# Optimization experiments

Hardware: AMD Instinct MI355X
Metric: run time of the kernel (lower is better)

## Reference

```python
import jax, jax.numpy as jnp
import numpy as np

GN_GROUPS = 32
GN_EPS = 1e-5


def conv3x3(x, w, b=None):
    # x: [B,C,H,W], w: [O,I,3,3]
    y = jax.lax.conv_general_dilated(x, w, (1, 1), 'SAME',
                                     dimension_numbers=('NCHW', 'OIHW', 'NCHW'))
    if b is not None:
        y = y + b[None, :, None, None]
    return y


def group_norm(x, gamma, beta):
    B, C, H, W = x.shape
    xg = x.reshape(B, GN_GROUPS, C // GN_GROUPS, H, W)
    mu = xg.mean(axis=(2, 3, 4), keepdims=True)
    var = ((xg - mu) ** 2).mean(axis=(2, 3, 4), keepdims=True)
    xn = ((xg - mu) * jax.lax.rsqrt(var + GN_EPS)).reshape(B, C, H, W)
    return xn * gamma[None, :, None, None] + beta[None, :, None, None]


def tower(x, ws, gammas, betas):
    # ws: [n_conv, C, C, 3, 3]; conv(bias=False) -> GroupNorm -> ReLU, n_conv times
    for i in range(ws.shape[0]):
        x = jax.nn.relu(group_norm(conv3x3(x, ws[i]), gammas[i], betas[i]))
    return x


def setup_inputs() -> dict:
    key = jax.random.key(0)
    ks = jax.random.split(key, 20)
    C, n_conv, n_fg = 256, 4, 20  # n_class - 1 = 20
    prior = 0.01
    B = 2
    sizes = [(100, 100), (50, 50), (25, 25), (13, 13), (7, 7)]
    inp = {}
    for i, (h, w) in enumerate(sizes):
        inp[f'feat{i}'] = jax.random.normal(ks[i], (B, C, h, w), dtype=jnp.float32)
    std = 0.01  # init_conv_std
    inp['cls_tw_w'] = std * jax.random.normal(ks[5], (n_conv, C, C, 3, 3), dtype=jnp.float32)
    inp['cls_tw_g'] = jnp.ones((n_conv, C), dtype=jnp.float32)
    inp['cls_tw_b'] = jnp.zeros((n_conv, C), dtype=jnp.float32)
    inp['box_tw_w'] = std * jax.random.normal(ks[6], (n_conv, C, C, 3, 3), dtype=jnp.float32)
    inp['box_tw_g'] = jnp.ones((n_conv, C), dtype=jnp.float32)
    inp['box_tw_b'] = jnp.zeros((n_conv, C), dtype=jnp.float32)
    inp['cls_pred_w'] = std * jax.random.normal(ks[7], (n_fg, C, 3, 3), dtype=jnp.float32)
    prior_bias = -np.log((1.0 - prior) / prior)
    inp['cls_pred_b'] = jnp.full((n_fg,), prior_bias, dtype=jnp.float32)
    inp['box_pred_w'] = std * jax.random.normal(ks[8], (4, C, 3, 3), dtype=jnp.float32)
    inp['box_pred_b'] = jnp.zeros((4,), dtype=jnp.float32)
    inp['ctr_pred_w'] = std * jax.random.normal(ks[9], (1, C, 3, 3), dtype=jnp.float32)
    inp['ctr_pred_b'] = jnp.zeros((1,), dtype=jnp.float32)
    inp['scales'] = jnp.ones((5,), dtype=jnp.float32)
    return inp


def reference(feat0, feat1, feat2, feat3, feat4,
              cls_tw_w, cls_tw_g, cls_tw_b,
              box_tw_w, box_tw_g, box_tw_b,
              cls_pred_w, cls_pred_b,
              box_pred_w, box_pred_b,
              ctr_pred_w, ctr_pred_b,
              scales):
    feats = [feat0, feat1, feat2, feat3, feat4]
    logits, bboxes, centers = [], [], []
    for i, feat in enumerate(feats):
        c = tower(feat, cls_tw_w, cls_tw_g, cls_tw_b)
        logits.append(conv3x3(c, cls_pred_w, cls_pred_b))
        centers.append(conv3x3(c, ctr_pred_w, ctr_pred_b))
        b = tower(feat, box_tw_w, box_tw_g, box_tw_b)
        bboxes.append(jnp.exp(conv3x3(b, box_pred_w, box_pred_b) * scales[i]))
    return tuple(logits + bboxes + centers)
```

## Files before the change

### kernel.cpp

```cpp
#include <hip/hip_runtime.h>
#include <hip/hip_bf16.h>
#include <cstdint>

typedef unsigned short u16;
typedef __attribute__((ext_vector_type(8))) short short8;
typedef __attribute__((ext_vector_type(4))) float floatx4;
typedef __attribute__((ext_vector_type(4))) int intx4;

#define PA_TOTAL 13696
#define CCH 256
#define KTOT 2304

struct Tables {
  int H[5], W[5], P[5], base[5], tile0[5];
  int lb[5], bb[5], cb[5];
};
struct FeatPtrs { const float* f[5]; };
struct ConvArgs {
  const u16* X[2];
  const u16* Wt[2];
  u16* outB[2];
  float* stats;
  float* dout;
  const float* biasCls; const float* biasCtr; const float* biasBox; const float* scales;
};
struct ReorderArgs {
  const float* cls_w; const float* box_w; const float* pcls_w; const float* ctr_w; const float* pbox_w;
  u16* wrCls; u16* wrBox; u16* wrPCls; u16* wrPBox;
};

__device__ __forceinline__ u16 f2bf(float f) {
  union { float f; unsigned u; } v; v.f = f;
  unsigned r = v.u + 0x7fffu + ((v.u >> 16) & 1u);
  return (u16)(r >> 16);
}
__device__ __forceinline__ float bf2f(u16 h) {
  union { unsigned u; float f; } v; v.u = ((unsigned)h) << 16;
  return v.f;
}

__device__ __forceinline__ void gload16(const void* g, void* l) {
  __builtin_amdgcn_global_load_lds(
      (const __attribute__((address_space(1))) void*)g,
      (__attribute__((address_space(3))) void*)l, 16, 0, 0);
}

__global__ void reorder_all(ReorderArgs ra) {
  __shared__ float row[KTOT];
  const int r = blockIdx.x;
  const float* s;
  u16* o;
  if (r < 1024)      { s = ra.cls_w  + (size_t)r * KTOT;          o = ra.wrCls  + (size_t)r * KTOT; }
  else if (r < 2048) { int q = r - 1024; s = ra.box_w  + (size_t)q * KTOT; o = ra.wrBox  + (size_t)q * KTOT; }
  else if (r < 2068) { int q = r - 2048; s = ra.pcls_w + (size_t)q * KTOT; o = ra.wrPCls + (size_t)q * KTOT; }
  else if (r == 2068){ s = ra.ctr_w;                               o = ra.wrPCls + (size_t)20 * KTOT; }
  else if (r < 2073) { int q = r - 2069; s = ra.pbox_w + (size_t)q * KTOT; o = ra.wrPBox + (size_t)q * KTOT; }
  else if (r < 2084) {
    u16* oz = ra.wrPCls + (size_t)(21 + (r - 2073)) * KTOT;
#pragma unroll
    for (int j = 0; j < 9; ++j) oz[threadIdx.x + j * 256] = 0;
    return;
  } else {
    u16* oz = ra.wrPBox + (size_t)(4 + (r - 2084)) * KTOT;
#pragma unroll
    for (int j = 0; j < 9; ++j) oz[threadIdx.x + j * 256] = 0;
    return;
  }
#pragma unroll
  for (int j = 0; j < 9; ++j) row[threadIdx.x + j * 256] = s[threadIdx.x + j * 256];
  __syncthreads();
#pragma unroll
  for (int j = 0; j < 9; ++j) {
    int k = threadIdx.x + j * 256;
    o[k] = f2bf(row[(k & 255) * 9 + (k >> 8)]);
  }
}

__global__ void convert_inputs(FeatPtrs fp, u16* __restrict__ out, Tables tb) {
  __shared__ float tile[32][33];
  const int pt = blockIdx.x, c32 = blockIdx.y, b = blockIdx.z;
  const int p0 = pt * 32;
  int lvl = 0;
#pragma unroll
  for (int i = 1; i < 5; ++i) if (p0 >= tb.base[i]) lvl = i;
  const int P = tb.P[lvl];
  const int pl0 = p0 - tb.base[lvl];
  const int r = threadIdx.x >> 5, col = threadIdx.x & 31;
  const float* src = fp.f[lvl] + ((size_t)b * CCH + c32 * 32) * P;
#pragma unroll
  for (int i = 0; i < 4; ++i) {
    int crow = r + i * 8;
    int pl = pl0 + col;
    tile[crow][col] = (pl < P) ? src[(size_t)crow * P + pl] : 0.f;
  }
  __syncthreads();
#pragma unroll
  for (int i = 0; i < 4; ++i) {
    int px = r + i * 8;
    out[((size_t)b * PA_TOTAL + p0 + px) * CCH + c32 * 32 + col] = f2bf(tile[col][px]);
  }
}

template <int MODE>
__global__ __launch_bounds__(256) void conv_mfma(ConvArgs a, Tables tb) {
  constexpr int NI = (MODE == 0) ? 4 : 1;
  constexpr int WROWS = (MODE == 0) ? 128 : 32;
  const int L = blockIdx.x + (MODE == 0 ? 107 : 108) * (blockIdx.y + 2 * blockIdx.z);
  const int xcd = L & 7, slot = L >> 3;
  int tower, mt, b, t;
  if (MODE == 0) {
    tower = xcd >> 2; mt = (xcd >> 1) & 1; b = xcd & 1; t = slot;
  } else {
    tower = xcd >> 2; mt = 0; b = (xcd >> 1) & 1; t = slot * 2 + (xcd & 1);
    if (t >= 107) return;
  }
  int lvl = 0;
#pragma unroll
  for (int i = 1; i < 5; ++i) if (t >= tb.tile0[i]) lvl = i;
  const int H = tb.H[lvl], W = tb.W[lvl], P = tb.P[lvl], base = tb.base[lvl];
  const int n0 = (t - tb.tile0[lvl]) * 128;

  const int tid = threadIdx.x;
  const int lane = tid & 63, wv = tid >> 6;
  const int wm = wv >> 1, wn = wv & 1;

  __shared__ u16 ldsAll[128 * 64 + WROWS * 64];
  u16* ldsX = ldsAll;
  u16* ldsW = ldsAll + 128 * 64;

  const u16* X = a.X[tower];
  const u16* Wt = a.Wt[tower];
  const char* Xb = (const char*)(X + ((size_t)b * PA_TOTAL + base) * CCH);
  const char* Wb = (const char*)(Wt + (size_t)(MODE == 0 ? mt * 128 : 0) * KTOT);

  const int qsw2 = ((lane & 7) ^ (lane >> 3)) * 16;
  int xoffG[4];
  unsigned mask9[4];
  int xlds[4];
#pragma unroll
  for (int t4 = 0; t4 < 4; ++t4) {
    int row = (t4 * 4 + wv) * 8 + (lane >> 3);
    int prow = n0 + row;
    int rr = prow / W, cc = prow - rr * W;
    unsigned m = 0;
#pragma unroll
    for (int tap = 0; tap < 9; ++tap) {
      const int dh = tap / 3 - 1, dw = tap % 3 - 1;
      bool v = ((unsigned)(rr + dh) < (unsigned)H) & ((unsigned)(cc + dw) < (unsigned)W);
      m |= ((unsigned)v) << tap;
    }
    mask9[t4] = m;
    xoffG[t4] = prow * (CCH * 2) + qsw2;
    xlds[t4] = (t4 * 4 + wv) * 1024;
  }
  const int padoff = P * (CCH * 2) + qsw2;
  int woffG[NI];
  int wlds[NI];
#pragma unroll
  for (int e = 0; e < NI; ++e) {
    int wrow = (MODE == 0) ? ((e * 4 + wv) * 8 + (lane >> 3)) : (wv * 8 + (lane >> 3));
    woffG[e] = wrow * (KTOT * 2) + qsw2;
    wlds[e] = 16384 + ((MODE == 0) ? ((e * 4 + wv) * 1024) : (wv * 1024));
  }

  const int arow = lane & 15, rsw = lane & 7, kq0 = lane >> 4;
  const int csw0 = (kq0 ^ rsw) * 8;
  int aoff[NI], boff[4];
#pragma unroll
  for (int i = 0; i < NI; ++i) {
    int rowb = (MODE == 0) ? (wm * 64 + i * 16) : (wm * 16);
    aoff[i] = (rowb + arow) * 64 + csw0;
  }
#pragma unroll
  for (int i = 0; i < 4; ++i) boff[i] = (wn * 64 + i * 16 + arow) * 64 + csw0;

  floatx4 acc[NI][4];
#pragma unroll
  for (int i = 0; i < NI; ++i)
#pragma unroll
    for (int j = 0; j < 4; ++j) acc[i][j] = (floatx4)0.f;

#pragma unroll 1
  for (int icb = 0; icb < 4; ++icb) {
#pragma unroll
    for (int tap = 0; tap < 9; ++tap) {
      __syncthreads();
      const int ko = (tap * 256 + icb * 64) * 2;
      const int dh = tap / 3 - 1, dw = tap % 3 - 1;
      const int doff = (dh * W + dw) * (CCH * 2) + icb * 128;
#pragma unroll
      for (int e = 0; e < NI; ++e)
        gload16(Wb + woffG[e] + ko, (char*)ldsAll + wlds[e]);
#pragma unroll
      for (int t4 = 0; t4 < 4; ++t4) {
        const int off = ((mask9[t4] >> tap) & 1u) ? (xoffG[t4] + doff) : padoff;
        gload16(Xb + off, (char*)ldsAll + xlds[t4]);
      }
      asm volatile("s_waitcnt vmcnt(0) lgkmcnt(0)\n\ts_barrier" ::: "memory");
      __builtin_amdgcn_s_setprio(1);
#pragma unroll
      for (int h = 0; h < 2; ++h) {
        const int hx = h * 32;
        short8 af[NI], bv[4];
#pragma unroll
        for (int i = 0; i < NI; ++i) af[i] = *(const short8*)(ldsW + (aoff[i] ^ hx));
#pragma unroll
        for (int j = 0; j < 4; ++j) bv[j] = *(const short8*)(ldsX + (boff[j] ^ hx));
#pragma unroll
        for (int i = 0; i < NI; ++i)
#pragma unroll
          for (int j = 0; j < 4; ++j)
            acc[i][j] = __builtin_amdgcn_mfma_f32_16x16x32_bf16(af[i], bv[j], acc[i][j], 0, 0, 0);
      }
      __builtin_amdgcn_s_setprio(0);
    }
  }

  const int quad = lane >> 4, col = lane & 15;
  if (MODE == 0) {
    u16* convB = a.outB[tower];
    float s[4] = {0.f, 0.f, 0.f, 0.f}, ss[4] = {0.f, 0.f, 0.f, 0.f};
#pragma unroll
    for (int j = 0; j < 4; ++j) {
      int pl = n0 + wn * 64 + j * 16 + col;
      bool valid = pl < P;
      u16* dst = convB + ((size_t)b * PA_TOTAL + base + pl) * CCH + mt * 128 + wm * 64 + quad * 4;
#pragma unroll
      for (int i = 0; i < 4; ++i) {
        ushort4 hv;
#pragma unroll
        for (int r = 0; r < 4; ++r) {
          u16 hh = f2bf(acc[i][j][r]);
          ((u16*)&hv)[r] = hh;
          float vr = bf2f(hh);
          if (valid) { s[i] += vr; ss[i] += vr * vr; }
        }
        if (valid) *(ushort4*)(dst + i * 16) = hv;
      }
    }
#pragma unroll
    for (int i = 0; i < 4; ++i) {
#pragma unroll
      for (int off = 16; off >= 1; off >>= 1) {
        s[i] += __shfl_down(s[i], off, 64);
        ss[i] += __shfl_down(ss[i], off, 64);
      }
    }
    if ((lane & 31) == 0) {
      int half = lane >> 5;
#pragma unroll
      for (int i = 0; i < 4; ++i) {
        float* st = a.stats + tower * 640 +
                    ((size_t)((b * 5 + lvl) * 32 + mt * 16 + wm * 8 + i * 2 + half)) * 2;
        atomicAdd(st, s[i]);
        atomicAdd(st + 1, ss[i]);
      }
    }
  } else {
    float* dout = a.dout;
    if (tower == 0) {
#pragma unroll
      for (int j = 0; j < 4; ++j) {
        int pl = n0 + wn * 64 + j * 16 + col;
        if (pl >= P) continue;
        int ocb = wm * 16 + quad * 4;
#pragma unroll
        for (int r = 0; r < 4; ++r) {
          int oc = ocb + r;
          float v = acc[0][j][r];
          if (oc < 20)       dout[tb.lb[lvl] + ((size_t)b * 20 + oc) * P + pl] = v + a.biasCls[oc];
          else if (oc == 20) dout[tb.cb[lvl] + (size_t)b * P + pl] = v + a.biasCtr[0];
        }
      }
    } else {
      float sc = a.scales[lvl];
#pragma unroll
      for (int j = 0; j < 4; ++j) {
        int pl = n0 + wn * 64 + j * 16 + col;
        if (pl >= P) continue;
        int ocb = wm * 16 + quad * 4;
#pragma unroll
        for (int r = 0; r < 4; ++r) {
          int oc = ocb + r;
          if (oc < 4)
            dout[tb.bb[lvl] + ((size_t)b * 4 + oc) * P + pl] = expf((acc[0][j][r] + a.biasBox[oc]) * sc);
        }
      }
    }
  }
}

__global__ void gn_norm(const u16* __restrict__ c0, const u16* __restrict__ c1,
                        const float* __restrict__ stats,
                        const float* __restrict__ g0, const float* __restrict__ b0,
                        const float* __restrict__ g1, const float* __restrict__ b1,
                        u16* __restrict__ a0, u16* __restrict__ a1, Tables tb) {
  const int tower = blockIdx.y;
  const u16* convB = tower ? c1 : c0;
  const float* gamma = tower ? g1 : g0;
  const float* beta = tower ? b1 : b0;
  u16* act = tower ? a1 : a0;
  int idx = blockIdx.x * 256 + threadIdx.x;
  int c8 = idx & 31;
  int rest = idx >> 5;
  int p = rest % PA_TOTAL;
  int b = rest / PA_TOTAL;
  int lvl = 0;
#pragma unroll
  for (int i = 1; i < 5; ++i) if (p >= tb.base[i]) lvl = i;
  if (p - tb.base[lvl] >= tb.P[lvl]) {
    short8 z = (short8)(short)0;
    *(short8*)(act + ((size_t)b * PA_TOTAL + p) * CCH + c8 * 8) = z;
    return;
  }
  const float* st = stats + tower * 640 + ((size_t)((b * 5 + lvl) * 32 + c8)) * 2;
  float cnt = 8.f * (float)tb.P[lvl];
  float mean = st[0] / cnt;
  float var = st[1] / cnt - mean * mean;
  float inv = rsqrtf(var + 1e-5f);
  const short8 x = *(const short8*)(convB + ((size_t)b * PA_TOTAL + p) * CCH + c8 * 8);
  short8 o;
#pragma unroll
  for (int j = 0; j < 8; ++j) {
    float v = bf2f((u16)x[j]);
    float y = (v - mean) * inv * gamma[c8 * 8 + j] + beta[c8 * 8 + j];
    y = fmaxf(y, 0.f);
    o[j] = (short)f2bf(y);
  }
  *(short8*)(act + ((size_t)b * PA_TOTAL + p) * CCH + c8 * 8) = o;
}

extern "C" void kernel_launch(void* const* d_in, const int* in_sizes, int n_in,
                              void* d_out, int out_size, void* d_ws, size_t ws_size,
                              hipStream_t stream) {
  const float* feat[5];
  for (int i = 0; i < 5; ++i) feat[i] = (const float*)d_in[i];
  const float* cls_tw_w  = (const float*)d_in[5];
  const float* cls_tw_g  = (const float*)d_in[6];
  const float* cls_tw_b  = (const float*)d_in[7];
  const float* box_tw_w  = (const float*)d_in[8];
  const float* box_tw_g  = (const float*)d_in[9];
  const float* box_tw_b  = (const float*)d_in[10];
  const float* cls_pred_w = (const float*)d_in[11];
  const float* cls_pred_b = (const float*)d_in[12];
  const float* box_pred_w = (const float*)d_in[13];
  const float* box_pred_b = (const float*)d_in[14];
  const float* ctr_pred_w = (const float*)d_in[15];
  const float* ctr_pred_b = (const float*)d_in[16];
  const float* scales     = (const float*)d_in[17];
  float* out = (float*)d_out;

  char* ws = (char*)d_ws;
  float* statsAll = (float*)(ws);
  u16*   WrCls  = (u16*)(ws + 24576);
  u16*   WrBox  = (u16*)(ws + 24576 + 4718592);
  u16*   WrPCls = (u16*)(ws + 24576 + 2 * 4718592);
  u16*   WrPBox = (u16*)(ws + 24576 + 2 * 4718592 + 147456);
  u16*   bufIn   = (u16*)(ws + 10625024);
  u16*   bufAct0 = (u16*)(ws + 10625024 + 1 * (size_t)14024704);
  u16*   bufAct1 = (u16*)(ws + 10625024 + 2 * (size_t)14024704);
  u16*   bufCv0  = (u16*)(ws + 10625024 + 3 * (size_t)14024704);
  u16*   bufCv1  = (u16*)(ws + 10625024 + 4 * (size_t)14024704);

  Tables tb = { {100,50,25,13,7}, {100,50,25,13,7}, {10000,2500,625,169,49},
                {0,10112,12672,13312,13568}, {0,79,99,104,106},
                {0,400000,500000,525000,531760},
                {533720,613720,633720,638720,640072},
                {640464,660464,665464,666714,667052} };

  hipMemsetAsync(statsAll, 0, 20480, stream);

  ReorderArgs ra = { cls_tw_w, box_tw_w, cls_pred_w, ctr_pred_w, box_pred_w,
                     WrCls, WrBox, WrPCls, WrPBox };
  reorder_all<<<2112, 256, 0, stream>>>(ra);

  FeatPtrs fp = {{feat[0], feat[1], feat[2], feat[3], feat[4]}};
  convert_inputs<<<dim3(PA_TOTAL / 32, 8, 2), 256, 0, stream>>>(fp, bufIn, tb);

  ConvArgs a;
  a.dout = out;
  a.biasCls = cls_pred_b; a.biasCtr = ctr_pred_b; a.biasBox = box_pred_b; a.scales = scales;
  a.outB[0] = bufCv0; a.outB[1] = bufCv1;

  for (int s = 0; s < 4; ++s) {
    a.X[0] = (s == 0) ? bufIn : bufAct0;
    a.X[1] = (s == 0) ? bufIn : bufAct1;
    a.Wt[0] = WrCls + (size_t)s * 256 * KTOT;
    a.Wt[1] = WrBox + (size_t)s * 256 * KTOT;
    a.stats = statsAll + (size_t)s * 1280;
    conv_mfma<0><<<dim3(107, 2, 4), 256, 0, stream>>>(a, tb);
    gn_norm<<<dim3(3424, 2), 256, 0, stream>>>(bufCv0, bufCv1, a.stats,
                                               cls_tw_g + s * 256, cls_tw_b + s * 256,
                                               box_tw_g + s * 256, box_tw_b + s * 256,
                                               bufAct0, bufAct1, tb);
  }
  a.X[0] = bufAct0; a.X[1] = bufAct1;
  a.Wt[0] = WrPCls; a.Wt[1] = WrPBox;
  conv_mfma<1><<<dim3(108, 2, 2), 256, 0, stream>>>(a, tb);
}
```

Baseline: 634.2 us.

## Reuse activation tile across horizontal taps in conv implicit GEMM

The activation tile is now loaded once per kernel row (136 pixel rows, covering a one-pixel halo on each side) instead of once per tap. The three horizontal taps read shifted rows from the same LDS tile. Horizontal border pixels are masked to zero in registers, and the bottom/top bounds are handled by clamping to the padding row. This cuts global activation loads and LDS writes by roughly a factor of three, at the cost of a slightly larger LDS buffer, extra masking ALU, and an uneven load split across waves.

```diff
diff --git a/kernel.cpp b/kernel.cpp
--- a/kernel.cpp
+++ b/kernel.cpp
@@ -104,7 +104,8 @@
 template <int MODE>
 __global__ __launch_bounds__(256) void conv_mfma(ConvArgs a, Tables tb) {
   constexpr int NI = (MODE == 0) ? 4 : 1;
-  constexpr int WROWS = (MODE == 0) ? 128 : 32;
+  constexpr int WBYTES = (MODE == 0) ? 16384 : 4096;
+  constexpr int XBYTES = 136 * 128;
   const int L = blockIdx.x + (MODE == 0 ? 107 : 108) * (blockIdx.y + 2 * blockIdx.z);
   const int xcd = L & 7, slot = L >> 3;
   int tower, mt, b, t;
@@ -117,62 +118,49 @@
   int lvl = 0;
 #pragma unroll
   for (int i = 1; i < 5; ++i) if (t >= tb.tile0[i]) lvl = i;
-  const int H = tb.H[lvl], W = tb.W[lvl], P = tb.P[lvl], base = tb.base[lvl];
+  const int W = tb.W[lvl], P = tb.P[lvl], base = tb.base[lvl];
   const int n0 = (t - tb.tile0[lvl]) * 128;
 
   const int tid = threadIdx.x;
   const int lane = tid & 63, wv = tid >> 6;
   const int wm = wv >> 1, wn = wv & 1;
 
-  __shared__ u16 ldsAll[128 * 64 + WROWS * 64];
+  __shared__ u16 ldsAll[(XBYTES + WBYTES) / 2];
   u16* ldsX = ldsAll;
-  u16* ldsW = ldsAll + 128 * 64;
-
-  const u16* X = a.X[tower];
-  const u16* Wt = a.Wt[tower];
-  const char* Xb = (const char*)(X + ((size_t)b * PA_TOTAL + base) * CCH);
-  const char* Wb = (const char*)(Wt + (size_t)(MODE == 0 ? mt * 128 : 0) * KTOT);
+  u16* ldsW = ldsAll + XBYTES / 2;
+
+  const char* Xb = (const char*)(a.X[tower] + ((size_t)b * PA_TOTAL + base) * CCH);
+  const char* Wb = (const char*)(a.Wt[tower] + (size_t)(MODE == 0 ? mt * 128 : 0) * KTOT);
 
   const int qsw2 = ((lane & 7) ^ (lane >> 3)) * 16;
-  int xoffG[4];
-  unsigned mask9[4];
-  int xlds[4];
-#pragma unroll
-  for (int t4 = 0; t4 < 4; ++t4) {
-    int row = (t4 * 4 + wv) * 8 + (lane >> 3);
-    int prow = n0 + row;
-    int rr = prow / W, cc = prow - rr * W;
-    unsigned m = 0;
-#pragma unroll
-    for (int tap = 0; tap < 9; ++tap) {
-      const int dh = tap / 3 - 1, dw = tap % 3 - 1;
-      bool v = ((unsigned)(rr + dh) < (unsigned)H) & ((unsigned)(cc + dw) < (unsigned)W);
-      m |= ((unsigned)v) << tap;
-    }
-    mask9[t4] = m;
-    xoffG[t4] = prow * (CCH * 2) + qsw2;
-    xlds[t4] = (t4 * 4 + wv) * 1024;
-  }
-  const int padoff = P * (CCH * 2) + qsw2;
-  int woffG[NI];
-  int wlds[NI];
+  const int rowbase = wv * 8 + (lane >> 3);
+  const int nxg = (wv == 0) ? 5 : 4;
+  int woffG[NI], wlds[NI];
 #pragma unroll
   for (int e = 0; e < NI; ++e) {
     int wrow = (MODE == 0) ? ((e * 4 + wv) * 8 + (lane >> 3)) : (wv * 8 + (lane >> 3));
     woffG[e] = wrow * (KTOT * 2) + qsw2;
-    wlds[e] = 16384 + ((MODE == 0) ? ((e * 4 + wv) * 1024) : (wv * 1024));
-  }
-
-  const int arow = lane & 15, rsw = lane & 7, kq0 = lane >> 4;
-  const int csw0 = (kq0 ^ rsw) * 8;
-  int aoff[NI], boff[4];
+    wlds[e] = XBYTES + ((MODE == 0) ? (e * 4 + wv) : wv) * 1024;
+  }
+
+  const int arow = lane & 15, kq0 = lane >> 4;
+  const int r7a = arow & 7;
+  int rbA[NI];
 #pragma unroll
   for (int i = 0; i < NI; ++i) {
     int rowb = (MODE == 0) ? (wm * 64 + i * 16) : (wm * 16);
-    aoff[i] = (rowb + arow) * 64 + csw0;
-  }
-#pragma unroll
-  for (int i = 0; i < 4; ++i) boff[i] = (wn * 64 + i * 16 + arow) * 64 + csw0;
+    rbA[i] = (rowb + arow) * 128;
+  }
+  int rbX[4];
+  int mL[4], mR[4];
+#pragma unroll
+  for (int j = 0; j < 4; ++j) {
+    int px = n0 + wn * 64 + j * 16 + arow;
+    rbX[j] = (wn * 64 + j * 16 + arow) * 128;
+    int cc = px % W;
+    mL[j] = (cc == 0) ? 0 : -1;
+    mR[j] = (cc == W - 1) ? 0 : -1;
+  }
 
   floatx4 acc[NI][4];
 #pragma unroll
@@ -182,37 +170,54 @@
 
 #pragma unroll 1
   for (int icb = 0; icb < 4; ++icb) {
-#pragma unroll
-    for (int tap = 0; tap < 9; ++tap) {
-      __syncthreads();
-      const int ko = (tap * 256 + icb * 64) * 2;
-      const int dh = tap / 3 - 1, dw = tap % 3 - 1;
-      const int doff = (dh * W + dw) * (CCH * 2) + icb * 128;
-#pragma unroll
-      for (int e = 0; e < NI; ++e)
-        gload16(Wb + woffG[e] + ko, (char*)ldsAll + wlds[e]);
-#pragma unroll
-      for (int t4 = 0; t4 < 4; ++t4) {
-        const int off = ((mask9[t4] >> tap) & 1u) ? (xoffG[t4] + doff) : padoff;
-        gload16(Xb + off, (char*)ldsAll + xlds[t4]);
-      }
-      asm volatile("s_waitcnt vmcnt(0) lgkmcnt(0)\n\ts_barrier" ::: "memory");
-      __builtin_amdgcn_s_setprio(1);
-#pragma unroll
-      for (int h = 0; h < 2; ++h) {
-        const int hx = h * 32;
-        short8 af[NI], bv[4];
-#pragma unroll
-        for (int i = 0; i < NI; ++i) af[i] = *(const short8*)(ldsW + (aoff[i] ^ hx));
-#pragma unroll
-        for (int j = 0; j < 4; ++j) bv[j] = *(const short8*)(ldsX + (boff[j] ^ hx));
-#pragma unroll
-        for (int i = 0; i < NI; ++i)
-#pragma unroll
-          for (int j = 0; j < 4; ++j)
-            acc[i][j] = __builtin_amdgcn_mfma_f32_16x16x32_bf16(af[i], bv[j], acc[i][j], 0, 0, 0);
-      }
-      __builtin_amdgcn_s_setprio(0);
+#pragma unroll 1
+    for (int dhi = 0; dhi < 3; ++dhi) {
+      const int dhW1 = (dhi - 1) * W - 1;
+#pragma unroll
+      for (int dwi = 0; dwi < 3; ++dwi) {
+        __syncthreads();
+        if (dwi == 0) {
+#pragma unroll
+          for (int k = 0; k < 5; ++k) {
+            if (k < nxg) {
+              const int q = n0 + dhW1 + rowbase + 32 * k;
+              const int qr = ((unsigned)q < (unsigned)P) ? q : P;
+              gload16(Xb + qr * 512 + icb * 128 + qsw2,
+                      (char*)ldsAll + (wv + 4 * k) * 1024);
+            }
+          }
+        }
+        const int ko = ((dhi * 3 + dwi) * 256 + icb * 64) * 2;
+#pragma unroll
+        for (int e = 0; e < NI; ++e)
+          gload16(Wb + woffG[e] + ko, (char*)ldsAll + wlds[e]);
+        asm volatile("s_waitcnt vmcnt(0) lgkmcnt(0)\n\ts_barrier" ::: "memory");
+        __builtin_amdgcn_s_setprio(1);
+        const int r7x = (arow + dwi) & 7;
+#pragma unroll
+        for (int h = 0; h < 2; ++h) {
+          const int cswA = ((h * 4 + kq0) ^ r7a) * 16;
+          const int cswX = ((h * 4 + kq0) ^ r7x) * 16;
+          short8 af[NI], bv[4];
+#pragma unroll
+          for (int i = 0; i < NI; ++i)
+            af[i] = *(const short8*)((const char*)ldsW + rbA[i] + cswA);
+#pragma unroll
+          for (int j = 0; j < 4; ++j) {
+            union { intx4 i4; short8 s8; } u;
+            u.i4 = *(const intx4*)((const char*)ldsX + rbX[j] + dwi * 128 + cswX);
+            if (dwi == 0) u.i4 &= (intx4)(mL[j]);
+            if (dwi == 2) u.i4 &= (intx4)(mR[j]);
+            bv[j] = u.s8;
+          }
+#pragma unroll
+          for (int i = 0; i < NI; ++i)
+#pragma unroll
+            for (int j = 0; j < 4; ++j)
+              acc[i][j] = __builtin_amdgcn_mfma_f32_16x16x32_bf16(af[i], bv[j], acc[i][j], 0, 0, 0);
+        }
+        __builtin_amdgcn_s_setprio(0);
+      }
     }
   }
 
```

New measurement: 652.7 us. 1.03x slower.
